# Kernel optimization log

Hardware: AMD Instinct MI355X
Metric: run time of the kernel (lower is better)

## Reference

```python
import jax, jax.numpy as jnp
import numpy as np

EPS = 1e-8

def _ternary(weight):
    # scale = mean(|W|); quantize to {-1,0,1}*scale with straight-through estimator
    scale = jnp.abs(weight).mean()
    w_norm = weight / jnp.maximum(scale, EPS)
    q = jnp.clip(jnp.round(w_norm), -1.0, 1.0) * scale
    # STE: forward value is q, gradient flows to `weight` as identity
    return weight + jax.lax.stop_gradient(q - weight)

def setup_inputs() -> dict:
    key = jax.random.key(0)
    k1, k2, k3 = jax.random.split(key, 3)
    B, S, D_IN, D_OUT = 8, 8192, 1024, 1024
    x = jax.random.normal(k1, (B, S, D_IN), dtype=jnp.float32)
    weight = jax.random.normal(k2, (D_OUT, D_IN), dtype=jnp.float32) * 0.02
    bias = jax.random.normal(k3, (D_OUT,), dtype=jnp.float32) * 0.01
    return {"x": x, "weight": weight, "bias": bias}

def reference(x, weight, bias):
    w_t = _ternary(weight)  # [out, in]
    # F.linear: x @ W^T + b
    return jnp.einsum('bsi,oi->bso', x, w_t) + bias
```

## Files before the change

### kernel.cpp

```cpp
#include <hip/hip_runtime.h>
#include <stdint.h>
#include <stddef.h>

typedef __bf16 bf16_t;
typedef __bf16 bf16x8 __attribute__((ext_vector_type(8)));
typedef __bf16 bf16x4 __attribute__((ext_vector_type(4)));
typedef float  f32x4  __attribute__((ext_vector_type(4)));

__global__ __launch_bounds__(256)
void k_abssum(const float* __restrict__ W, float* __restrict__ partials) {
    const int t = threadIdx.x;
    const int b = blockIdx.x;
    const f32x4* W4 = reinterpret_cast<const f32x4*>(W);
    float s = 0.f;
    const int base = b * 1024 + t;
#pragma unroll
    for (int i = 0; i < 4; ++i) {
        f32x4 v = W4[base + i * 256];
        s += fabsf(v[0]) + fabsf(v[1]) + fabsf(v[2]) + fabsf(v[3]);
    }
#pragma unroll
    for (int off = 32; off > 0; off >>= 1) s += __shfl_down(s, off);
    __shared__ float red[4];
    if ((t & 63) == 0) red[t >> 6] = s;
    __syncthreads();
    if (t == 0) partials[b] = red[0] + red[1] + red[2] + red[3];
}

__global__ __launch_bounds__(256)
void k_ternarize(const float* __restrict__ W, const float* __restrict__ partials,
                 bf16_t* __restrict__ T, float* __restrict__ scale_out) {
    const int t = threadIdx.x;
    float s = partials[t];
#pragma unroll
    for (int off = 32; off > 0; off >>= 1) s += __shfl_down(s, off);
    __shared__ float red[4];
    if ((t & 63) == 0) red[t >> 6] = s;
    __syncthreads();
    const float total = red[0] + red[1] + red[2] + red[3];
    const float scale = total * (1.0f / 1048576.0f);
    const float inv   = 1.0f / fmaxf(scale, 1e-8f);

    const int c  = blockIdx.x * 256 + t;
    const int n  = c >> 7;
    const int k  = (c & 127) * 8;
    const float* wp = W + (size_t)n * 1024 + k;
    f32x4 w0 = *reinterpret_cast<const f32x4*>(wp);
    f32x4 w1 = *reinterpret_cast<const f32x4*>(wp + 4);
    bf16x8 q;
#pragma unroll
    for (int j = 0; j < 4; ++j) {
        float q0 = fminf(1.f, fmaxf(-1.f, rintf(w0[j] * inv)));
        float q1 = fminf(1.f, fmaxf(-1.f, rintf(w1[j] * inv)));
        q[j]     = (bf16_t)q0;
        q[4 + j] = (bf16_t)q1;
    }
    const int bn = n >> 7, nn = n & 127;
    const int kt = k >> 6, kq8 = (k & 63) >> 3;
    const size_t chunk = ((size_t)(bn * 16 + kt) * 8 + kq8) * 128 + nn;
    reinterpret_cast<bf16x8*>(T)[chunk] = q;
    if (c == 0) scale_out[0] = scale;
}

__global__ __launch_bounds__(256, 3)
void k_gemm(const float* __restrict__ X, const bf16_t* __restrict__ T,
            const float* __restrict__ bias, const float* __restrict__ scale_p,
            float* __restrict__ Out) {
    __shared__ bf16_t As[8192];
    __shared__ bf16_t Bs[8192];

    const int tid  = threadIdx.x;
    const int lane = tid & 63;
    const int w    = tid >> 6;
    const int wr   = w >> 1;
    const int wc   = w & 1;
    const int lq   = lane >> 4;
    const int rl   = lane & 15;

    const int bid  = blockIdx.x;
    const int sid  = (bid & 7) * 512 + (bid >> 3);
    const int bn   = sid & 7;
    const int bm   = sid >> 3;
    const int row0 = bm * 128;
    const int col0 = bn * 128;

    const int am  = tid >> 3;
    const int akq = tid & 7;
    const float* xA = X + (size_t)(row0 + am) * 1024 + akq * 8;
    int awoff[4];
#pragma unroll
    for (int h = 0; h < 4; ++h) {
        const int m = am + 32 * h;
        awoff[h] = (akq * 128 + (m & ~7) + ((m + akq) & 7)) * 16;
    }

    const bf16_t* gB = T + (size_t)bn * 16 * 8192 + (size_t)(w * 4) * 512 + (size_t)lane * 8;
    bf16_t* ldsB = Bs + (size_t)(w * 4) * 512;

    int aoff[2][4], boff[2][4];
#pragma unroll
    for (int kk = 0; kk < 2; ++kk) {
        const int kq8 = kk * 4 + lq;
#pragma unroll
        for (int i = 0; i < 4; ++i) {
            const int m = wr * 64 + i * 16 + rl;
            aoff[kk][i] = (kq8 * 128 + (m & ~7) + ((m + kq8) & 7)) * 16;
            boff[kk][i] = (kq8 * 128 + wc * 64 + i * 16 + rl) * 16;
        }
    }

    f32x4 acc[4][4];
    {
        f32x4 z = {0.f, 0.f, 0.f, 0.f};
#pragma unroll
        for (int i = 0; i < 4; ++i)
#pragma unroll
            for (int j = 0; j < 4; ++j) acc[i][j] = z;
    }

    f32x4 a0[4], a1[4];
#define LOAD_A(kt)                                                          \
    {                                                                       \
        _Pragma("unroll")                                                   \
        for (int h = 0; h < 4; ++h) {                                       \
            const float* p = xA + (size_t)h * 32 * 1024 + (kt) * 64;        \
            a0[h] = *(const f32x4*)(p);                                     \
            a1[h] = *(const f32x4*)(p + 4);                                 \
        }                                                                   \
    }

    LOAD_A(0);

    for (int kt = 0; kt < 16; ++kt) {
        __syncthreads();
#pragma unroll
        for (int i = 0; i < 4; ++i)
            __builtin_amdgcn_global_load_lds(
                (const __attribute__((address_space(1))) void*)(gB + (size_t)kt * 8192 + i * 512),
                (__attribute__((address_space(3))) void*)(ldsB + i * 512), 16, 0, 0);
#pragma unroll
        for (int h = 0; h < 4; ++h) {
            bf16x8 v;
#pragma unroll
            for (int j = 0; j < 4; ++j) {
                v[j]     = (bf16_t)a0[h][j];
                v[4 + j] = (bf16_t)a1[h][j];
            }
            *reinterpret_cast<bf16x8*>((char*)As + awoff[h]) = v;
        }
        __syncthreads();

        if (kt + 1 < 16) LOAD_A(kt + 1);

#pragma unroll
        for (int kk = 0; kk < 2; ++kk) {
            bf16x8 af[4], bfr[4];
#pragma unroll
            for (int i = 0; i < 4; ++i) {
                af[i]  = *reinterpret_cast<const bf16x8*>((const char*)As + aoff[kk][i]);
                bfr[i] = *reinterpret_cast<const bf16x8*>((const char*)Bs + boff[kk][i]);
            }
#pragma unroll
            for (int mi = 0; mi < 4; ++mi)
#pragma unroll
                for (int ni = 0; ni < 4; ++ni)
                    acc[mi][ni] = __builtin_amdgcn_mfma_f32_16x16x32_bf16(
                        af[mi], bfr[ni], acc[mi][ni], 0, 0, 0);
        }
    }

    const float scale = scale_p[0];
    float bv[4];
#pragma unroll
    for (int ni = 0; ni < 4; ++ni)
        bv[ni] = bias[col0 + wc * 64 + ni * 16 + rl];
#pragma unroll
    for (int mi = 0; mi < 4; ++mi) {
        const int gm0 = row0 + wr * 64 + mi * 16 + lq * 4;
#pragma unroll
        for (int ni = 0; ni < 4; ++ni) {
            const int gn = col0 + wc * 64 + ni * 16 + rl;
#pragma unroll
            for (int j = 0; j < 4; ++j)
                Out[(size_t)(gm0 + j) * 1024 + gn] = acc[mi][ni][j] * scale + bv[ni];
        }
    }
#undef LOAD_A
}

extern "C" void kernel_launch(void* const* d_in, const int* in_sizes, int n_in,
                              void* d_out, int out_size, void* d_ws, size_t ws_size,
                              hipStream_t stream) {
    const float* x    = (const float*)d_in[0];
    const float* W    = (const float*)d_in[1];
    const float* bias = (const float*)d_in[2];
    float* out = (float*)d_out;

    float*  ws_part  = (float*)d_ws;
    float*  ws_scale = ws_part + 256;
    bf16_t* ws_T     = (bf16_t*)(ws_part + 512);

    hipLaunchKernelGGL(k_abssum,    dim3(256), dim3(256), 0, stream, W, ws_part);
    hipLaunchKernelGGL(k_ternarize, dim3(512), dim3(256), 0, stream, W, ws_part, ws_T, ws_scale);
    hipLaunchKernelGGL(k_gemm,      dim3(4096), dim3(256), 0, stream, x, ws_T, bias, ws_scale, out);
}
```

Baseline: 576.1 us.

## Load A fragments directly from global into registers, double-buffer B in LDS

Drops LDS staging for the fp32 activation tile. Each wave now loads its own A fragments straight from global memory into MFMA operand registers and converts them to bf16 there. The B (ternary weight) tile is double-buffered in LDS, so the next k-tile is prefetched while the current one computes, and one barrier per iteration is removed. The trade-off is that A is no longer shared across the two column waves, which doubles global/L2 traffic for X. The A loads also sit right before the MFMAs with little latency hiding, and the per-lane load pattern is less coalesced.

```diff
diff --git a/kernel.cpp b/kernel.cpp
--- a/kernel.cpp
+++ b/kernel.cpp
@@ -66,8 +66,7 @@
 void k_gemm(const float* __restrict__ X, const bf16_t* __restrict__ T,
             const float* __restrict__ bias, const float* __restrict__ scale_p,
             float* __restrict__ Out) {
-    __shared__ bf16_t As[8192];
-    __shared__ bf16_t Bs[8192];
+    __shared__ bf16_t Bs[2][8192];
 
     const int tid  = threadIdx.x;
     const int lane = tid & 63;
@@ -84,30 +83,17 @@
     const int row0 = bm * 128;
     const int col0 = bn * 128;
 
-    const int am  = tid >> 3;
-    const int akq = tid & 7;
-    const float* xA = X + (size_t)(row0 + am) * 1024 + akq * 8;
-    int awoff[4];
+    const bf16_t* gB = T + (size_t)bn * 16 * 8192 + (size_t)(w * 4) * 512 + (size_t)lane * 8;
+    const int ldsBoff = w * 4 * 512;
+
+    const float* xbase = X + (size_t)(row0 + wr * 64 + rl) * 1024 + lq * 8;
+
+    int boff[2][4];
 #pragma unroll
-    for (int h = 0; h < 4; ++h) {
-        const int m = am + 32 * h;
-        awoff[h] = (akq * 128 + (m & ~7) + ((m + akq) & 7)) * 16;
-    }
-
-    const bf16_t* gB = T + (size_t)bn * 16 * 8192 + (size_t)(w * 4) * 512 + (size_t)lane * 8;
-    bf16_t* ldsB = Bs + (size_t)(w * 4) * 512;
-
-    int aoff[2][4], boff[2][4];
+    for (int kk = 0; kk < 2; ++kk)
 #pragma unroll
-    for (int kk = 0; kk < 2; ++kk) {
-        const int kq8 = kk * 4 + lq;
-#pragma unroll
-        for (int i = 0; i < 4; ++i) {
-            const int m = wr * 64 + i * 16 + rl;
-            aoff[kk][i] = (kq8 * 128 + (m & ~7) + ((m + kq8) & 7)) * 16;
-            boff[kk][i] = (kq8 * 128 + wc * 64 + i * 16 + rl) * 16;
-        }
-    }
+        for (int i = 0; i < 4; ++i)
+            boff[kk][i] = ((kk * 4 + lq) * 128 + wc * 64 + i * 16 + rl) * 16;
 
     f32x4 acc[4][4];
     {
@@ -118,48 +104,43 @@
             for (int j = 0; j < 4; ++j) acc[i][j] = z;
     }
 
-    f32x4 a0[4], a1[4];
-#define LOAD_A(kt)                                                          \
-    {                                                                       \
-        _Pragma("unroll")                                                   \
-        for (int h = 0; h < 4; ++h) {                                       \
-            const float* p = xA + (size_t)h * 32 * 1024 + (kt) * 64;        \
-            a0[h] = *(const f32x4*)(p);                                     \
-            a1[h] = *(const f32x4*)(p + 4);                                 \
-        }                                                                   \
-    }
-
-    LOAD_A(0);
+#pragma unroll
+    for (int i = 0; i < 4; ++i)
+        __builtin_amdgcn_global_load_lds(
+            (const __attribute__((address_space(1))) void*)(gB + i * 512),
+            (__attribute__((address_space(3))) void*)(&Bs[0][ldsBoff + i * 512]), 16, 0, 0);
+    __syncthreads();
 
     for (int kt = 0; kt < 16; ++kt) {
-        __syncthreads();
+        const int cur = kt & 1;
+        if (kt + 1 < 16) {
 #pragma unroll
-        for (int i = 0; i < 4; ++i)
-            __builtin_amdgcn_global_load_lds(
-                (const __attribute__((address_space(1))) void*)(gB + (size_t)kt * 8192 + i * 512),
-                (__attribute__((address_space(3))) void*)(ldsB + i * 512), 16, 0, 0);
-#pragma unroll
-        for (int h = 0; h < 4; ++h) {
-            bf16x8 v;
-#pragma unroll
-            for (int j = 0; j < 4; ++j) {
-                v[j]     = (bf16_t)a0[h][j];
-                v[4 + j] = (bf16_t)a1[h][j];
-            }
-            *reinterpret_cast<bf16x8*>((char*)As + awoff[h]) = v;
+            for (int i = 0; i < 4; ++i)
+                __builtin_amdgcn_global_load_lds(
+                    (const __attribute__((address_space(1))) void*)(gB + (size_t)(kt + 1) * 8192 + i * 512),
+                    (__attribute__((address_space(3))) void*)(&Bs[cur ^ 1][ldsBoff + i * 512]), 16, 0, 0);
         }
-        __syncthreads();
-
-        if (kt + 1 < 16) LOAD_A(kt + 1);
-
+        const char* bbase = (const char*)&Bs[cur][0];
 #pragma unroll
         for (int kk = 0; kk < 2; ++kk) {
+            f32x4 r0[4], r1[4];
+#pragma unroll
+            for (int mi = 0; mi < 4; ++mi) {
+                const float* p = xbase + (size_t)mi * 16384 + kt * 64 + kk * 32;
+                r0[mi] = *(const f32x4*)(p);
+                r1[mi] = *(const f32x4*)(p + 4);
+            }
             bf16x8 af[4], bfr[4];
 #pragma unroll
-            for (int i = 0; i < 4; ++i) {
-                af[i]  = *reinterpret_cast<const bf16x8*>((const char*)As + aoff[kk][i]);
-                bfr[i] = *reinterpret_cast<const bf16x8*>((const char*)Bs + boff[kk][i]);
-            }
+            for (int mi = 0; mi < 4; ++mi)
+#pragma unroll
+                for (int j = 0; j < 4; ++j) {
+                    af[mi][j]     = (bf16_t)r0[mi][j];
+                    af[mi][4 + j] = (bf16_t)r1[mi][j];
+                }
+#pragma unroll
+            for (int ni = 0; ni < 4; ++ni)
+                bfr[ni] = *reinterpret_cast<const bf16x8*>(bbase + boff[kk][ni]);
 #pragma unroll
             for (int mi = 0; mi < 4; ++mi)
 #pragma unroll
@@ -167,6 +148,7 @@
                     acc[mi][ni] = __builtin_amdgcn_mfma_f32_16x16x32_bf16(
                         af[mi], bfr[ni], acc[mi][ni], 0, 0, 0);
         }
+        __syncthreads();
     }
 
     const float scale = scale_p[0];
@@ -185,7 +167,6 @@
                 Out[(size_t)(gm0 + j) * 1024 + gn] = acc[mi][ni][j] * scale + bv[ni];
         }
     }
-#undef LOAD_A
 }
 
 extern "C" void kernel_launch(void* const* d_in, const int* in_sizes, int n_in,
```

New measurement: 880.6 us. 52.9% more time.
